# Performance work log

Measured on AMD Instinct MI355X. Metric: run time of the kernel, lower is better.

Reference implementation:

```python
import jax, jax.numpy as jnp
import numpy as np

B, T, C = 2, 2048, 1024
H = 16
D = C // H
EPS = 1e-5


def _layernorm(x, g, b):
    mu = jnp.mean(x, axis=-1, keepdims=True)
    var = jnp.mean(jnp.square(x - mu), axis=-1, keepdims=True)
    return (x - mu) * jax.lax.rsqrt(var + EPS) * g + b


def setup_inputs() -> dict:
    key = jax.random.key(0)
    ks = jax.random.split(key, 8)
    s = lambda fan_in: 1.0 / np.sqrt(fan_in)
    return {
        "x": jax.random.normal(ks[0], (B, T, C), dtype=jnp.float32),
        "ln1_g": jnp.ones((C,), jnp.float32),
        "ln1_b": jnp.zeros((C,), jnp.float32),
        "w_qkv": jax.random.uniform(ks[1], (C, 3 * C), jnp.float32, -s(C), s(C)),
        "b_qkv": jnp.zeros((3 * C,), jnp.float32),
        "w_attn_proj": jax.random.uniform(ks[2], (C, C), jnp.float32, -s(C), s(C)),
        "b_attn_proj": jnp.zeros((C,), jnp.float32),
        "ln2_g": jnp.ones((C,), jnp.float32),
        "ln2_b": jnp.zeros((C,), jnp.float32),
        "w_fc": jax.random.uniform(ks[3], (C, 4 * C), jnp.float32, -s(C), s(C)),
        "b_fc": jnp.zeros((4 * C,), jnp.float32),
        "w_out": jax.random.uniform(ks[4], (4 * C, C), jnp.float32, -s(4 * C), s(4 * C)),
        "b_out": jnp.zeros((C,), jnp.float32),
    }


def reference(x, ln1_g, ln1_b, w_qkv, b_qkv, w_attn_proj, b_attn_proj,
              ln2_g, ln2_b, w_fc, b_fc, w_out, b_out):
    # --- masked multi-head attention on ln1(x) ---
    h = _layernorm(x, ln1_g, ln1_b)
    qkv = h @ w_qkv + b_qkv                      # [B,T,3C]
    q, k, v = jnp.split(qkv, 3, axis=-1)
    q = q.reshape(B, T, H, D)
    k = k.reshape(B, T, H, D)
    v = v.reshape(B, T, H, D)
    # NOTE: source scales by emb_dim**-0.5 (not head_dim**-0.5) — kept faithful.
    wei = jnp.einsum('bqhd,bkhd->bhqk', q, k) * (C ** -0.5)
    causal = jnp.tril(jnp.ones((T, T), dtype=bool))
    wei = jnp.where(causal, wei, -jnp.inf)
    attn = jax.nn.softmax(wei, axis=-1)
    out = jnp.einsum('bhqk,bkhd->bqhd', attn, v).reshape(B, T, C)
    x = x + out @ w_attn_proj + b_attn_proj
    # --- GELU MLP on ln2(x) ---
    h = _layernorm(x, ln2_g, ln2_b)
    h = jax.nn.gelu(h @ w_fc + b_fc, approximate=False)
    return x + h @ w_out + b_out
```

## Files before the change

kernel.cpp:

```cpp
#include <hip/hip_runtime.h>
#include <hip/hip_bf16.h>
#include <math.h>

#define BB 2
#define TT 2048
#define CC 1024
#define HH 16
#define DD 64
#define EPS 1e-5f

typedef __bf16 bf16x8 __attribute__((ext_vector_type(8)));
typedef float f32x4 __attribute__((ext_vector_type(4)));

struct alignas(8) bf4 { __bf16 v[4]; };

__device__ __forceinline__ void gld16(const void* g, void* l) {
    __builtin_amdgcn_global_load_lds(
        (const __attribute__((address_space(1))) void*)g,
        (__attribute__((address_space(3))) void*)l, 16, 0, 0);
}

__device__ __forceinline__ f32x4 mfma16(bf16x8 a, bf16x8 b, f32x4 c) {
    return __builtin_amdgcn_mfma_f32_16x16x32_bf16(a, b, c, 0, 0, 0);
}

__global__ __launch_bounds__(256) void wt_cvt_kernel(const float* __restrict__ w,
                                                     __bf16* __restrict__ wt,
                                                     int K, int N) {
    __shared__ float tile[32][33];
    const int tx = threadIdx.x & 31, ty = threadIdx.x >> 5;
    const int k0 = blockIdx.x * 32, n0 = blockIdx.y * 32;
    #pragma unroll
    for (int i = 0; i < 4; ++i)
        tile[ty + i * 8][tx] = w[(size_t)(k0 + ty + i * 8) * N + n0 + tx];
    __syncthreads();
    #pragma unroll
    for (int i = 0; i < 4; ++i)
        wt[(size_t)(n0 + ty + i * 8) * K + k0 + tx] = (__bf16)tile[tx][ty + i * 8];
}

__global__ __launch_bounds__(256) void ln_kernel(const float* __restrict__ x,
                                                 const float* __restrict__ gg,
                                                 const float* __restrict__ bb,
                                                 __bf16* __restrict__ out) {
    __shared__ float red[4];
    __shared__ float red2[4];
    const int row = blockIdx.x;
    const int t = threadIdx.x;
    const float4 v = *(const float4*)(x + (size_t)row * CC + t * 4);

    float s = v.x + v.y + v.z + v.w;
    #pragma unroll
    for (int o = 32; o; o >>= 1) s += __shfl_down(s, o);
    const int lane = t & 63, w = t >> 6;
    if (lane == 0) red[w] = s;
    __syncthreads();
    const float mu = (red[0] + red[1] + red[2] + red[3]) * (1.0f / CC);

    const float dx = v.x - mu, dy = v.y - mu, dz = v.z - mu, dw = v.w - mu;
    float s2 = dx * dx + dy * dy + dz * dz + dw * dw;
    #pragma unroll
    for (int o = 32; o; o >>= 1) s2 += __shfl_down(s2, o);
    if (lane == 0) red2[w] = s2;
    __syncthreads();
    const float var = (red2[0] + red2[1] + red2[2] + red2[3]) * (1.0f / CC);
    const float rstd = rsqrtf(var + EPS);

    const float4 g4 = *(const float4*)(gg + t * 4);
    const float4 b4 = *(const float4*)(bb + t * 4);
    bf4 o4;
    o4.v[0] = (__bf16)(dx * rstd * g4.x + b4.x);
    o4.v[1] = (__bf16)(dy * rstd * g4.y + b4.y);
    o4.v[2] = (__bf16)(dz * rstd * g4.z + b4.z);
    o4.v[3] = (__bf16)(dw * rstd * g4.w + b4.w);
    *(bf4*)(out + (size_t)row * CC + t * 4) = o4;
}

template <int BN, int MODE>
__global__ __launch_bounds__(256) void mfma_gemm(const __bf16* __restrict__ A,
                                                 const __bf16* __restrict__ Bt,
                                                 const float* __restrict__ bias,
                                                 const float* __restrict__ resid,
                                                 void* __restrict__ Cv,
                                                 void* __restrict__ Cv2,
                                                 int M, int N, int K) {
    constexpr int NT = BN / 32;
    __shared__ __bf16 As[128 * 64];
    __shared__ __bf16 Bs[BN * 64];
    const int t = threadIdx.x;
    const int w = t >> 6, lane = t & 63;
    const int quad = lane >> 4, ln = lane & 15;
    const int m0 = blockIdx.y * 128, n0 = blockIdx.x * BN;
    const int wm = (w >> 1) * 64, wn = (w & 1) * (BN / 2);

    f32x4 acc[4][NT];
    #pragma unroll
    for (int im = 0; im < 4; ++im)
        #pragma unroll
        for (int in = 0; in < NT; ++in) acc[im][in] = (f32x4){0.f, 0.f, 0.f, 0.f};

    const int srow = t >> 3;
    const int scol = ((t & 7) ^ (srow & 7)) << 3;
    const __bf16* gA = A + (size_t)(m0 + srow) * K + scol;
    const __bf16* gB = Bt + (size_t)(n0 + srow) * K + scol;
    __bf16* lA = &As[t * 8];
    __bf16* lB = &Bs[t * 8];

    for (int k0 = 0; k0 < K; k0 += 64) {
        __syncthreads();
        #pragma unroll
        for (int j = 0; j < 4; ++j)
            gld16(gA + k0 + (size_t)(j * 32) * K, lA + j * 2048);
        #pragma unroll
        for (int j = 0; j < BN / 32; ++j)
            gld16(gB + k0 + (size_t)(j * 32) * K, lB + j * 2048);
        __syncthreads();

        #pragma unroll
        for (int half = 0; half < 2; ++half) {
            bf16x8 af[4], bfr[NT];
            #pragma unroll
            for (int im = 0; im < 4; ++im)
                af[im] = *(const bf16x8*)&As[(wm + im * 16 + ln) * 64 +
                                             (((half * 4 + quad) ^ (ln & 7)) << 3)];
            #pragma unroll
            for (int in = 0; in < NT; ++in)
                bfr[in] = *(const bf16x8*)&Bs[(wn + in * 16 + ln) * 64 +
                                              (((half * 4 + quad) ^ (ln & 7)) << 3)];
            #pragma unroll
            for (int im = 0; im < 4; ++im)
                #pragma unroll
                for (int in = 0; in < NT; ++in)
                    acc[im][in] = mfma16(af[im], bfr[in], acc[im][in]);
        }
    }

    if (MODE == 5 && n0 >= 2 * CC) {
        __syncthreads();
        __bf16* scr = Bs + w * (16 * 70);
        const int bq = m0 >> 11;
        const int tbase = (m0 & 2047) + wm;
        const int dly = lane >> 2;
        const int seg = lane & 3;
        #pragma unroll
        for (int in = 0; in < 4; ++in) {
            const int col = n0 + wn + in * 16 + ln;
            const float bv = bias[col];
            #pragma unroll
            for (int im = 0; im < 4; ++im)
                #pragma unroll
                for (int r = 0; r < 4; ++r)
                    scr[ln * 70 + im * 16 + (quad << 2) + r] =
                        (__bf16)(acc[im][in][r] + bv);
            const int dg = (n0 - 2 * CC) + wn + in * 16 + dly;
            __bf16* dst = (__bf16*)Cv2 +
                ((size_t)((bq * HH + (dg >> 6)) * DD + (dg & 63))) * TT +
                tbase + seg * 16;
            *(bf16x8*)dst = *(const bf16x8*)&scr[dly * 70 + seg * 16];
            *(bf16x8*)(dst + 8) = *(const bf16x8*)&scr[dly * 70 + seg * 16 + 8];
        }
    } else {
        #pragma unroll
        for (int in = 0; in < NT; ++in) {
            const int col = n0 + wn + in * 16 + ln;
            const float bv = bias[col];
            #pragma unroll
            for (int im = 0; im < 4; ++im) {
                const int row = m0 + wm + im * 16 + (quad << 2);
                if (MODE == 5) {
                    #pragma unroll
                    for (int r = 0; r < 4; ++r)
                        ((__bf16*)Cv)[(size_t)(row + r) * (2 * CC) + col] =
                            (__bf16)(acc[im][in][r] + bv);
                } else {
                    #pragma unroll
                    for (int r = 0; r < 4; ++r) {
                        float v = acc[im][in][r] + bv;
                        const size_t off = (size_t)(row + r) * N + col;
                        if (MODE == 2) {
                            v = 0.5f * v * (1.0f + erff(v * 0.70710678118654752f));
                            ((__bf16*)Cv)[off] = (__bf16)v;
                        } else if (MODE == 1) {
                            ((float*)Cv)[off] = v + resid[off];
                        }
                    }
                }
            }
        }
    }
}

#define PSTR 72

__global__ __launch_bounds__(256) void flash_mfma_kernel(
    const __bf16* __restrict__ qk,
    const __bf16* __restrict__ vT,
    __bf16* __restrict__ out) {
    __shared__ __bf16 Ks[2][64 * 64];
    __shared__ __bf16 Vs[2][64 * 64];
    __shared__ __bf16 Ps[4][16 * PSTR];

    const int px = blockIdx.x;
    const int h = blockIdx.y, b = blockIdx.z;
    const int t = threadIdx.x;
    const int w = t >> 6, lane = t & 63;
    const int quad = lane >> 4, ln = lane & 15;
    const float scale = 0.03125f;

    const int pc0 = t, pc1 = t + 256;
    const int rr0 = pc0 >> 3, c0 = (pc0 & 7) ^ (rr0 & 7);
    const int rr1 = pc1 >> 3, c1 = (pc1 & 7) ^ (rr1 & 7);
    const __bf16* gK0 = qk + (size_t)(b * TT + rr0) * (2 * CC) + CC + h * DD + c0 * 8;
    const __bf16* gK1 = qk + (size_t)(b * TT + rr1) * (2 * CC) + CC + h * DD + c1 * 8;
    const __bf16* gV0 = vT + ((size_t)((b * HH + h) * DD) + rr0) * TT + c0 * 8;
    const __bf16* gV1 = vT + ((size_t)((b * HH + h) * DD) + rr1) * TT + c1 * 8;

    #pragma unroll
    for (int phase = 0; phase < 2; ++phase) {
        const int qt = phase ? px : (31 - px);

        const size_t qrow = (size_t)(b * TT + qt * 64 + w * 16 + ln);
        const bf16x8 qf0 = *(const bf16x8*)&qk[qrow * (2 * CC) + h * DD + quad * 8];
        const bf16x8 qf1 = *(const bf16x8*)&qk[qrow * (2 * CC) + h * DD + 32 + quad * 8];

        f32x4 oacc[4];
        #pragma unroll
        for (int nd = 0; nd < 4; ++nd) oacc[nd] = (f32x4){0.f, 0.f, 0.f, 0.f};
        f32x4 lacc = (f32x4){0.f, 0.f, 0.f, 0.f};

        __syncthreads();
        gld16(gK0, &Ks[0][pc0 * 8]);
        gld16(gK1, &Ks[0][pc1 * 8]);
        gld16(gV0, &Vs[0][pc0 * 8]);
        gld16(gV1, &Vs[0][pc1 * 8]);

        int cur = 0;
        for (int kt = 0; kt <= qt; ++kt) {
            __syncthreads();
            if (kt < qt) {
                const int nx = cur ^ 1;
                const size_t ko = (size_t)(kt + 1) * 64 * (2 * CC);
                const int vo = (kt + 1) * 64;
                gld16(gK0 + ko, &Ks[nx][pc0 * 8]);
                gld16(gK1 + ko, &Ks[nx][pc1 * 8]);
                gld16(gV0 + vo, &Vs[nx][pc0 * 8]);
                gld16(gV1 + vo, &Vs[nx][pc1 * 8]);
            }

            const int ntmax = (kt == qt) ? w : 3;

            f32x4 p[4];
            #pragma unroll
            for (int nt = 0; nt < 4; ++nt) {
                if (nt <= ntmax) {
                    const bf16x8 kf0 = *(const bf16x8*)
                        &Ks[cur][(nt * 16 + ln) * 64 + ((quad ^ (ln & 7)) << 3)];
                    const bf16x8 kf1 = *(const bf16x8*)
                        &Ks[cur][(nt * 16 + ln) * 64 + (((4 + quad) ^ (ln & 7)) << 3)];
                    f32x4 z = (f32x4){0.f, 0.f, 0.f, 0.f};
                    z = mfma16(qf0, kf0, z);
                    z = mfma16(qf1, kf1, z);
                    #pragma unroll
                    for (int r = 0; r < 4; ++r) {
                        float pv = __expf(z[r] * scale);
                        if (kt == qt && nt == ntmax && ln > quad * 4 + r) pv = 0.f;
                        p[nt][r] = pv;
                    }
                } else {
                    p[nt] = (f32x4){0.f, 0.f, 0.f, 0.f};
                }
            }

            #pragma unroll
            for (int r = 0; r < 4; ++r)
                lacc[r] += (p[0][r] + p[1][r]) + (p[2][r] + p[3][r]);

            #pragma unroll
            for (int nt = 0; nt < 4; ++nt)
                #pragma unroll
                for (int r = 0; r < 4; ++r)
                    Ps[w][(quad * 4 + r) * PSTR + nt * 16 + ln] = (__bf16)p[nt][r];

            const bf16x8 pf0 = *(const bf16x8*)&Ps[w][ln * PSTR + quad * 8];
            const bf16x8 pf1 = *(const bf16x8*)&Ps[w][ln * PSTR + 32 + quad * 8];
            #pragma unroll
            for (int nd = 0; nd < 4; ++nd) {
                const bf16x8 vf0 = *(const bf16x8*)
                    &Vs[cur][(nd * 16 + ln) * 64 + ((quad ^ (ln & 7)) << 3)];
                const bf16x8 vf1 = *(const bf16x8*)
                    &Vs[cur][(nd * 16 + ln) * 64 + (((4 + quad) ^ (ln & 7)) << 3)];
                oacc[nd] = mfma16(pf0, vf0, oacc[nd]);
                oacc[nd] = mfma16(pf1, vf1, oacc[nd]);
            }
            cur ^= 1;
        }

        float lr[4];
        #pragma unroll
        for (int r = 0; r < 4; ++r) {
            lr[r] = lacc[r];
            #pragma unroll
            for (int off = 1; off < 16; off <<= 1)
                lr[r] += __shfl_xor(lr[r], off);
        }

        #pragma unroll
        for (int r = 0; r < 4; ++r) {
            const float inv = 1.0f / lr[r];
            const size_t orow = (size_t)(b * TT + qt * 64 + w * 16 + quad * 4 + r);
            #pragma unroll
            for (int nd = 0; nd < 4; ++nd)
                out[orow * CC + h * DD + nd * 16 + ln] = (__bf16)(oacc[nd][r] * inv);
        }
    }
}

extern "C" void kernel_launch(void* const* d_in, const int* in_sizes, int n_in,
                              void* d_out, int out_size, void* d_ws, size_t ws_size,
                              hipStream_t stream) {
    const float* x       = (const float*)d_in[0];
    const float* ln1_g   = (const float*)d_in[1];
    const float* ln1_b   = (const float*)d_in[2];
    const float* w_qkv   = (const float*)d_in[3];
    const float* b_qkv   = (const float*)d_in[4];
    const float* w_proj  = (const float*)d_in[5];
    const float* b_proj  = (const float*)d_in[6];
    const float* ln2_g   = (const float*)d_in[7];
    const float* ln2_b   = (const float*)d_in[8];
    const float* w_fc    = (const float*)d_in[9];
    const float* b_fc    = (const float*)d_in[10];
    const float* w_out   = (const float*)d_in[11];
    const float* b_out   = (const float*)d_in[12];
    float* out = (float*)d_out;

    char* ws = (char*)d_ws;
    const size_t MB = 1024ull * 1024ull;
    __bf16* h_bf   = (__bf16*)(ws + 0);
    __bf16* wqkvT  = (__bf16*)(ws + 8 * MB);
    __bf16* wprojT = (__bf16*)(ws + 14 * MB);
    __bf16* wfcT   = (__bf16*)(ws + 16 * MB);
    __bf16* woutT  = (__bf16*)(ws + 24 * MB);
    __bf16* qk_bf  = (__bf16*)(ws + 32 * MB);
    __bf16* vT     = (__bf16*)(ws + 48 * MB);
    __bf16* attn   = (__bf16*)(ws + 56 * MB);
    float*  x2     = (float*)(ws + 64 * MB);
    __bf16* fc_out = (__bf16*)(ws + 32 * MB);

    const int M = BB * TT;

    wt_cvt_kernel<<<dim3(32, 96), 256, 0, stream>>>(w_qkv, wqkvT, CC, 3 * CC);
    wt_cvt_kernel<<<dim3(32, 32), 256, 0, stream>>>(w_proj, wprojT, CC, CC);
    wt_cvt_kernel<<<dim3(32, 128), 256, 0, stream>>>(w_fc, wfcT, CC, 4 * CC);
    wt_cvt_kernel<<<dim3(128, 32), 256, 0, stream>>>(w_out, woutT, 4 * CC, CC);

    ln_kernel<<<M, 256, 0, stream>>>(x, ln1_g, ln1_b, h_bf);
    mfma_gemm<128, 5><<<dim3(3 * CC / 128, M / 128), 256, 0, stream>>>(
        h_bf, wqkvT, b_qkv, nullptr, qk_bf, vT, M, 3 * CC, CC);
    flash_mfma_kernel<<<dim3(TT / 128, HH, BB), 256, 0, stream>>>(qk_bf, vT, attn);
    mfma_gemm<64, 1><<<dim3(CC / 64, M / 128), 256, 0, stream>>>(
        attn, wprojT, b_proj, x, x2, nullptr, M, CC, CC);
    ln_kernel<<<M, 256, 0, stream>>>(x2, ln2_g, ln2_b, h_bf);
    mfma_gemm<128, 2><<<dim3(4 * CC / 128, M / 128), 256, 0, stream>>>(
        h_bf, wfcT, b_fc, nullptr, fc_out, nullptr, M, 4 * CC, CC);
    mfma_gemm<64, 1><<<dim3(CC / 64, M / 128), 256, 0, stream>>>(
        fc_out, woutT, b_out, x2, out, nullptr, M, CC, 4 * CC);
}
```

Baseline: 371.8 us.

## Double-buffer GEMM K-tiles with single barrier and use fast erf approximation in GELU

The GEMM main loop now uses K-tiles of 32 instead of 64 and keeps two LDS buffers. The next tile's global-to-LDS loads are issued before computing on the current one, leaving one barrier per iteration instead of two. This is meant to overlap memory latency with MFMA work, at the cost of more loop iterations and a new XOR swizzle pattern for the narrower tile. Separately, erff in the GELU epilogue is replaced by an Abramowitz–Stegun polynomial using a fast reciprocal and __expf, which trades a small amount of accuracy for cheaper epilogue math.

```diff
diff --git a/kernel.cpp b/kernel.cpp
--- a/kernel.cpp
+++ b/kernel.cpp
@@ -22,6 +22,21 @@
 
 __device__ __forceinline__ f32x4 mfma16(bf16x8 a, bf16x8 b, f32x4 c) {
     return __builtin_amdgcn_mfma_f32_16x16x32_bf16(a, b, c, 0, 0, 0);
+}
+
+__device__ __forceinline__ float gelu_exact(float v) {
+    const float y = v * 0.70710678118654752f;
+    const float ax = fabsf(y);
+    const float t = __builtin_amdgcn_rcpf(fmaf(0.3275911f, ax, 1.0f));
+    const float e = __expf(-ax * ax);
+    float p = fmaf(1.061405429f, t, -1.453152027f);
+    p = fmaf(p, t, 1.421413741f);
+    p = fmaf(p, t, -0.284496736f);
+    p = fmaf(p, t, 0.254829592f);
+    p = p * t;
+    float r = fmaf(-p, e, 1.0f);
+    r = (y < 0.0f) ? -r : r;
+    return 0.5f * v * (1.0f + r);
 }
 
 __global__ __launch_bounds__(256) void wt_cvt_kernel(const float* __restrict__ w,
@@ -85,8 +100,9 @@
                                                  void* __restrict__ Cv2,
                                                  int M, int N, int K) {
     constexpr int NT = BN / 32;
-    __shared__ __bf16 As[128 * 64];
-    __shared__ __bf16 Bs[BN * 64];
+    constexpr int BSTR = BN * 32;
+    __shared__ __bf16 As[2 * 128 * 32];
+    __shared__ __bf16 Bs[2 * BSTR];
     const int t = threadIdx.x;
     const int w = t >> 6, lane = t & 63;
     const int quad = lane >> 4, ln = lane & 15;
@@ -99,45 +115,47 @@
         #pragma unroll
         for (int in = 0; in < NT; ++in) acc[im][in] = (f32x4){0.f, 0.f, 0.f, 0.f};
 
-    const int srow = t >> 3;
-    const int scol = ((t & 7) ^ (srow & 7)) << 3;
+    const int srow = t >> 2;
+    const int scol = ((t & 3) ^ ((t >> 3) & 3)) << 3;
     const __bf16* gA = A + (size_t)(m0 + srow) * K + scol;
     const __bf16* gB = Bt + (size_t)(n0 + srow) * K + scol;
-    __bf16* lA = &As[t * 8];
-    __bf16* lB = &Bs[t * 8];
-
-    for (int k0 = 0; k0 < K; k0 += 64) {
+
+    gld16(gA, &As[t * 8]);
+    gld16(gA + (size_t)64 * K, &As[2048 + t * 8]);
+    gld16(gB, &Bs[t * 8]);
+    if (BN == 128) gld16(gB + (size_t)64 * K, &Bs[2048 + t * 8]);
+
+    const int rsw = (quad ^ ((ln >> 1) & 3)) << 3;
+
+    int cur = 0;
+    for (int k0 = 0; k0 < K; k0 += 32) {
         __syncthreads();
-        #pragma unroll
-        for (int j = 0; j < 4; ++j)
-            gld16(gA + k0 + (size_t)(j * 32) * K, lA + j * 2048);
-        #pragma unroll
-        for (int j = 0; j < BN / 32; ++j)
-            gld16(gB + k0 + (size_t)(j * 32) * K, lB + j * 2048);
-        __syncthreads();
-
-        #pragma unroll
-        for (int half = 0; half < 2; ++half) {
-            bf16x8 af[4], bfr[NT];
-            #pragma unroll
-            for (int im = 0; im < 4; ++im)
-                af[im] = *(const bf16x8*)&As[(wm + im * 16 + ln) * 64 +
-                                             (((half * 4 + quad) ^ (ln & 7)) << 3)];
+        if (k0 + 32 < K) {
+            const int nx = cur ^ 1;
+            gld16(gA + k0 + 32, &As[nx * 4096 + t * 8]);
+            gld16(gA + k0 + 32 + (size_t)64 * K, &As[nx * 4096 + 2048 + t * 8]);
+            gld16(gB + k0 + 32, &Bs[nx * BSTR + t * 8]);
+            if (BN == 128)
+                gld16(gB + k0 + 32 + (size_t)64 * K, &Bs[nx * BSTR + 2048 + t * 8]);
+        }
+        bf16x8 af[4], bfr[NT];
+        #pragma unroll
+        for (int im = 0; im < 4; ++im)
+            af[im] = *(const bf16x8*)&As[cur * 4096 + (wm + im * 16 + ln) * 32 + rsw];
+        #pragma unroll
+        for (int in = 0; in < NT; ++in)
+            bfr[in] = *(const bf16x8*)&Bs[cur * BSTR + (wn + in * 16 + ln) * 32 + rsw];
+        #pragma unroll
+        for (int im = 0; im < 4; ++im)
             #pragma unroll
             for (int in = 0; in < NT; ++in)
-                bfr[in] = *(const bf16x8*)&Bs[(wn + in * 16 + ln) * 64 +
-                                              (((half * 4 + quad) ^ (ln & 7)) << 3)];
-            #pragma unroll
-            for (int im = 0; im < 4; ++im)
-                #pragma unroll
-                for (int in = 0; in < NT; ++in)
-                    acc[im][in] = mfma16(af[im], bfr[in], acc[im][in]);
-        }
+                acc[im][in] = mfma16(af[im], bfr[in], acc[im][in]);
+        cur ^= 1;
     }
 
     if (MODE == 5 && n0 >= 2 * CC) {
         __syncthreads();
-        __bf16* scr = Bs + w * (16 * 70);
+        __bf16* scr = As + w * (16 * 70);
         const int bq = m0 >> 11;
         const int tbase = (m0 & 2047) + wm;
         const int dly = lane >> 2;
@@ -167,22 +185,17 @@
             #pragma unroll
             for (int im = 0; im < 4; ++im) {
                 const int row = m0 + wm + im * 16 + (quad << 2);
-                if (MODE == 5) {
-                    #pragma unroll
-                    for (int r = 0; r < 4; ++r)
-                        ((__bf16*)Cv)[(size_t)(row + r) * (2 * CC) + col] =
-                            (__bf16)(acc[im][in][r] + bv);
-                } else {
-                    #pragma unroll
-                    for (int r = 0; r < 4; ++r) {
-                        float v = acc[im][in][r] + bv;
+                #pragma unroll
+                for (int r = 0; r < 4; ++r) {
+                    float v = acc[im][in][r] + bv;
+                    if (MODE == 5) {
+                        ((__bf16*)Cv)[(size_t)(row + r) * (2 * CC) + col] = (__bf16)v;
+                    } else if (MODE == 2) {
+                        v = gelu_exact(v);
+                        ((__bf16*)Cv)[(size_t)(row + r) * N + col] = (__bf16)v;
+                    } else {
                         const size_t off = (size_t)(row + r) * N + col;
-                        if (MODE == 2) {
-                            v = 0.5f * v * (1.0f + erff(v * 0.70710678118654752f));
-                            ((__bf16*)Cv)[off] = (__bf16)v;
-                        } else if (MODE == 1) {
-                            ((float*)Cv)[off] = v + resid[off];
-                        }
+                        ((float*)Cv)[off] = v + resid[off];
                     }
                 }
             }
```

Measured after the change: 378.0 us. About the same (+1.7%).
